# Kernel optimization log

Hardware: AMD Instinct MI355X
Metric: run time of the kernel (lower is better)

The kernel has to match this reference:

```python
import jax, jax.numpy as jnp
import numpy as np

N_NODES = 50000
N_EDGES = 800000
C_IN = 128
C_OUT = 64
C_HID = 2 * C_OUT  # 128


def setup_inputs() -> dict:
    key = jax.random.key(0)
    ks = jax.random.split(key, 8)
    x = jax.random.normal(ks[0], (N_NODES, C_IN), dtype=jnp.float32)
    edge_index = jax.random.randint(ks[1], (2, N_EDGES), 0, N_NODES, dtype=jnp.int64)
    s1 = 1.0 / np.sqrt(C_IN)
    s2 = 1.0 / np.sqrt(C_HID)
    s3 = 1.0 / np.sqrt(C_OUT)
    W1 = jax.random.uniform(ks[2], (C_IN, C_HID), jnp.float32, -s1, s1)
    b1 = jnp.zeros((C_HID,), jnp.float32)
    W2 = jax.random.uniform(ks[3], (C_HID, C_OUT), jnp.float32, -s2, s2)
    b2 = jnp.zeros((C_OUT,), jnp.float32)
    Wb = jax.random.uniform(ks[4], (1, C_OUT, C_OUT), jnp.float32, -s3, s3)
    bb = jax.random.uniform(ks[5], (1,), jnp.float32, -s3, s3)
    return {"x": x, "edge_index": edge_index, "W1": W1, "b1": b1,
            "W2": W2, "b2": b2, "Wb": Wb, "bb": bb}


def gcn_conv(x, W, b, src, dst, n_nodes):
    # PyG GCNConv: h = x @ W; add self-loops; symmetric normalization D^-1/2 (A+I) D^-1/2.
    h = x @ W  # [N, F]
    ones = jnp.ones((src.shape[0],), h.dtype)
    deg = jax.ops.segment_sum(ones, dst, num_segments=n_nodes) + 1.0  # +1 for self-loop
    dinv = jax.lax.rsqrt(deg)
    norm = dinv[src] * dinv[dst]  # [E]
    msgs = h[src] * norm[:, None]  # [E, F]
    agg = jax.ops.segment_sum(msgs, dst, num_segments=n_nodes)
    # self-loop contribution: norm_ii = 1/deg_i
    agg = agg + h * (1.0 / deg)[:, None]
    return agg + b


def reference(x, edge_index, W1, b1, W2, b2, Wb, bb):
    src = edge_index[0]
    dst = edge_index[1]
    n = x.shape[0]
    # encode
    h = jax.nn.relu(gcn_conv(x, W1, b1, src, dst, n))
    z = gcn_conv(h, W2, b2, src, dst, n)  # [N, C_OUT]
    # decode: bilinear on (z[src], z[dst]) -> sigmoid
    zs = z[src]  # [E, C_OUT]
    zd = z[dst]  # [E, C_OUT]
    logits = jnp.einsum('ec,ocd,ed->eo', zs, Wb, zd) + bb  # [E, 1]
    return jax.nn.sigmoid(logits)
```

## Files before the change

### kernel.cpp

```cpp
#include <hip/hip_runtime.h>
#include <hip/hip_bf16.h>


#define N_NODES 50000
#define BSH 7
#define BSZ 128
#define NBUCK ((N_NODES + BSZ - 1) / BSZ)
#define EPB 4096
#define CAP 3072

typedef unsigned int u32;
typedef unsigned short u16;

typedef __attribute__((ext_vector_type(8))) short bf16x8;
typedef __attribute__((ext_vector_type(4))) float f32x4;
union frag_u { bf16x8 f; u32 u[4]; uint4 v; };

__device__ __forceinline__ float bflo(u32 u) { return __uint_as_float(u << 16); }
__device__ __forceinline__ float bfhi(u32 u) { return __uint_as_float(u & 0xffff0000u); }
__device__ __forceinline__ u32 f2bf(float f) {
    u32 b = __float_as_uint(f);
    return (b + 0x7fffu + ((b >> 16) & 1u)) >> 16;
}
__device__ __forceinline__ u32 pack2(float a, float b) { return f2bf(a) | (f2bf(b) << 16); }

__global__ __launch_bounds__(256) void gemm1_scatter(
        const float* __restrict__ X, const float* __restrict__ W,
        u16* __restrict__ O, int n_rows, int gblk,
        const int* __restrict__ src, const int* __restrict__ dst,
        int* __restrict__ bcur, u32* __restrict__ pair, int E) {
    constexpr int K = 128, NOUT = 128;
    constexpr int KP = K + 8;
    constexpr int NT = NOUT / 16;
    constexpr int KS = K / 32;
    __shared__ __align__(16) char smem[NOUT * KP * 2 * sizeof(u16)];
    int t = threadIdx.x;

    if ((int)blockIdx.x < gblk) {
        u16* Wt_hi = (u16*)smem;
        u16* Wt_lo = Wt_hi + NOUT * KP;
        for (int i4 = t; i4 < K * NOUT / 4; i4 += 256) {
            int k = (i4 * 4) / NOUT;
            int n0 = (i4 * 4) % NOUT;
            float4 w4 = *(const float4*)&W[(size_t)k * NOUT + n0];
            float wv[4] = {w4.x, w4.y, w4.z, w4.w};
#pragma unroll
            for (int q = 0; q < 4; q++) {
                u32 hi = f2bf(wv[q]);
                u32 lo = f2bf(wv[q] - bflo(hi));
                Wt_hi[(n0 + q) * KP + k] = (u16)hi;
                Wt_lo[(n0 + q) * KP + k] = (u16)lo;
            }
        }
        __syncthreads();

        int wave = t >> 6;
        int lane = t & 63;
        int m16 = lane & 15;
        int quad = lane >> 4;
        int row0 = blockIdx.x * 128 + wave * 32;

        f32x4 acc[2][NT] = {};
        for (int ks = 0; ks < KS; ks++) {
            frag_u a_hi[2], a_lo[2];
#pragma unroll
            for (int mt = 0; mt < 2; mt++) {
                int row = row0 + mt * 16 + m16;
                row = row < n_rows ? row : n_rows - 1;
                const float* Xp = X + (size_t)row * K + ks * 32 + quad * 8;
                float4 x0 = *(const float4*)Xp;
                float4 x1 = *(const float4*)(Xp + 4);
                float xv[8] = {x0.x, x0.y, x0.z, x0.w, x1.x, x1.y, x1.z, x1.w};
#pragma unroll
                for (int p = 0; p < 4; p++) {
                    u32 h0 = f2bf(xv[2 * p]), h1 = f2bf(xv[2 * p + 1]);
                    a_hi[mt].u[p] = h0 | (h1 << 16);
                    a_lo[mt].u[p] = pack2(xv[2 * p] - bflo(h0), xv[2 * p + 1] - bflo(h1));
                }
            }
#pragma unroll
            for (int nt = 0; nt < NT; nt++) {
                int n = nt * 16 + m16;
                frag_u b_hi, b_lo;
                b_hi.v = *(const uint4*)&Wt_hi[n * KP + ks * 32 + quad * 8];
                b_lo.v = *(const uint4*)&Wt_lo[n * KP + ks * 32 + quad * 8];
#pragma unroll
                for (int mt = 0; mt < 2; mt++) {
                    acc[mt][nt] = __builtin_amdgcn_mfma_f32_16x16x32_bf16(a_hi[mt].f, b_hi.f, acc[mt][nt], 0, 0, 0);
                    acc[mt][nt] = __builtin_amdgcn_mfma_f32_16x16x32_bf16(a_hi[mt].f, b_lo.f, acc[mt][nt], 0, 0, 0);
                    acc[mt][nt] = __builtin_amdgcn_mfma_f32_16x16x32_bf16(a_lo[mt].f, b_hi.f, acc[mt][nt], 0, 0, 0);
                }
            }
        }
#pragma unroll
        for (int mt = 0; mt < 2; mt++)
#pragma unroll
            for (int nt = 0; nt < NT; nt++)
#pragma unroll
                for (int r = 0; r < 4; r++) {
                    int row = row0 + mt * 16 + quad * 4 + r;
                    if (row < n_rows)
                        O[(size_t)row * NOUT + nt * 16 + m16] = (u16)f2bf(acc[mt][nt][r]);
                }
    } else {
        int* hist = (int*)smem;
        for (int i = t; i < NBUCK; i += 256) hist[i] = 0;
        __syncthreads();
        int base = ((int)blockIdx.x - gblk) * EPB;
        int s_[16], d_[16];
#pragma unroll
        for (int it = 0; it < 16; it++) {
            int e = base + it * 256 + t;
            if (e < E) {
                s_[it] = src[e];
                d_[it] = dst[e];
                atomicAdd(&hist[d_[it] >> BSH], 1);
            } else {
                d_[it] = -1;
            }
        }
        __syncthreads();
        for (int b = t; b < NBUCK; b += 256) {
            int c = hist[b];
            hist[b] = c ? (b * CAP + atomicAdd(&bcur[b], c)) : 0;
        }
        __syncthreads();
#pragma unroll
        for (int it = 0; it < 16; it++) {
            if (d_[it] >= 0) {
                int b = d_[it] >> BSH;
                int off = atomicAdd(&hist[b], 1);
                pair[off] = (u32)s_[it] | ((u32)(d_[it] & (BSZ - 1)) << 16);
            }
        }
    }
}

__global__ __launch_bounds__(256) void bucket_sort(const u32* __restrict__ pair,
                                                   const int* __restrict__ bcur,
                                                   int* __restrict__ row_ptr,
                                                   int* __restrict__ col,
                                                   float* __restrict__ dinv,
                                                   float* __restrict__ inv, int n, int E) {
    __shared__ int ssum[256];
    __shared__ int cnt[BSZ];
    __shared__ int scn[BSZ];
    __shared__ int cur[BSZ];
    int t = threadIdx.x;
    int base = blockIdx.x << BSH;
    int nn = min(BSZ, n - base);
    int accp = 0;
    for (int i = t; i < (int)blockIdx.x; i += 256) accp += bcur[i];
    ssum[t] = accp;
    __syncthreads();
    for (int s = 128; s > 0; s >>= 1) {
        if (t < s) ssum[t] += ssum[t + s];
        __syncthreads();
    }
    int b0 = ssum[0];
    int cntE = bcur[blockIdx.x];
    int p0 = blockIdx.x * CAP;
    if (t < BSZ) cnt[t] = 0;
    __syncthreads();
    for (int j = t; j < cntE; j += 256)
        atomicAdd(&cnt[pair[p0 + j] >> 16], 1);
    __syncthreads();
    if (t < BSZ) scn[t] = cnt[t];
    __syncthreads();
    for (int off = 1; off < BSZ; off <<= 1) {
        int a = (t < BSZ && t >= off) ? scn[t - off] : 0;
        __syncthreads();
        if (t < BSZ) scn[t] += a;
        __syncthreads();
    }
    if (t < nn) {
        int excl = b0 + scn[t] - cnt[t];
        row_ptr[base + t] = excl;
        cur[t] = excl;
        float d = (float)cnt[t] + 1.0f;
        dinv[base + t] = rsqrtf(d);
        inv[base + t] = 1.0f / d;
    }
    if (t == 0 && blockIdx.x == NBUCK - 1) row_ptr[n] = E;
    __syncthreads();
    for (int j = t; j < cntE; j += 256) {
        u32 p = pair[p0 + j];
        int ln = (int)(p >> 16);
        int pos = atomicAdd(&cur[ln], 1);
        col[pos] = (int)(p & 0xffffu);
    }
}

template <int K, int NOUT>
__global__ __launch_bounds__(256) void gemm_mfma_bf(const u16* __restrict__ Xv,
                                                    const float* __restrict__ W,
                                                    u16* __restrict__ O, int n_rows) {
    constexpr int KP = K + 8;
    constexpr int NT = NOUT / 16;
    constexpr int KS = K / 32;
    __shared__ __align__(16) u16 Wt_hi[NOUT * KP];
    __shared__ __align__(16) u16 Wt_lo[NOUT * KP];
    int t = threadIdx.x;
    for (int i4 = t; i4 < K * NOUT / 4; i4 += 256) {
        int k = (i4 * 4) / NOUT;
        int n0 = (i4 * 4) % NOUT;
        float4 w4 = *(const float4*)&W[(size_t)k * NOUT + n0];
        float wv[4] = {w4.x, w4.y, w4.z, w4.w};
#pragma unroll
        for (int q = 0; q < 4; q++) {
            u32 hi = f2bf(wv[q]);
            u32 lo = f2bf(wv[q] - bflo(hi));
            Wt_hi[(n0 + q) * KP + k] = (u16)hi;
            Wt_lo[(n0 + q) * KP + k] = (u16)lo;
        }
    }
    __syncthreads();

    int wave = t >> 6;
    int lane = t & 63;
    int m16 = lane & 15;
    int quad = lane >> 4;
    int row0 = blockIdx.x * 128 + wave * 32;

    f32x4 acc[2][NT] = {};
    for (int ks = 0; ks < KS; ks++) {
        frag_u a_hi[2];
#pragma unroll
        for (int mt = 0; mt < 2; mt++) {
            int row = row0 + mt * 16 + m16;
            row = row < n_rows ? row : n_rows - 1;
            a_hi[mt].v = *(const uint4*)(Xv + (size_t)row * K + ks * 32 + quad * 8);
        }
#pragma unroll
        for (int nt = 0; nt < NT; nt++) {
            int n = nt * 16 + m16;
            frag_u b_hi, b_lo;
            b_hi.v = *(const uint4*)&Wt_hi[n * KP + ks * 32 + quad * 8];
            b_lo.v = *(const uint4*)&Wt_lo[n * KP + ks * 32 + quad * 8];
#pragma unroll
            for (int mt = 0; mt < 2; mt++) {
                acc[mt][nt] = __builtin_amdgcn_mfma_f32_16x16x32_bf16(a_hi[mt].f, b_hi.f, acc[mt][nt], 0, 0, 0);
                acc[mt][nt] = __builtin_amdgcn_mfma_f32_16x16x32_bf16(a_hi[mt].f, b_lo.f, acc[mt][nt], 0, 0, 0);
            }
        }
    }
#pragma unroll
    for (int mt = 0; mt < 2; mt++)
#pragma unroll
        for (int nt = 0; nt < NT; nt++)
#pragma unroll
            for (int r = 0; r < 4; r++) {
                int row = row0 + mt * 16 + quad * 4 + r;
                if (row < n_rows)
                    O[(size_t)row * NOUT + nt * 16 + m16] = (u16)f2bf(acc[mt][nt][r]);
            }
}

template <int C, bool RELU>
__global__ __launch_bounds__(256) void agg_pull(const u16* __restrict__ H,
                                                const int* __restrict__ row_ptr,
                                                const int* __restrict__ col,
                                                const float* __restrict__ dinv,
                                                const float* __restrict__ inv,
                                                const float* __restrict__ b,
                                                u16* __restrict__ O, int n) {
    constexpr int TPN = C / 8;
    const uint4* Hv = (const uint4*)H;
    int tid = blockIdx.x * 256 + threadIdx.x;
    int node = tid / TPN;
    if (node >= n) return;
    int part = tid % TPN;
    int c8 = part * 8;
    float dn = dinv[node];
    float iv = inv[node];
    float acc[8];
    {
        uint4 h = Hv[(size_t)node * TPN + part];
        acc[0] = bflo(h.x) * iv + b[c8 + 0];
        acc[1] = bfhi(h.x) * iv + b[c8 + 1];
        acc[2] = bflo(h.y) * iv + b[c8 + 2];
        acc[3] = bfhi(h.y) * iv + b[c8 + 3];
        acc[4] = bflo(h.z) * iv + b[c8 + 4];
        acc[5] = bfhi(h.z) * iv + b[c8 + 5];
        acc[6] = bflo(h.w) * iv + b[c8 + 6];
        acc[7] = bfhi(h.w) * iv + b[c8 + 7];
    }
    int j = row_ptr[node];
    int end = row_ptr[node + 1];
    for (; j + 3 < end; j += 4) {
        int s0 = col[j], s1 = col[j + 1], s2 = col[j + 2], s3 = col[j + 3];
        float n0 = dn * dinv[s0], n1 = dn * dinv[s1];
        float n2 = dn * dinv[s2], n3 = dn * dinv[s3];
        uint4 v0 = Hv[(size_t)s0 * TPN + part];
        uint4 v1 = Hv[(size_t)s1 * TPN + part];
        uint4 v2 = Hv[(size_t)s2 * TPN + part];
        uint4 v3 = Hv[(size_t)s3 * TPN + part];
        acc[0] += bflo(v0.x) * n0 + bflo(v1.x) * n1 + bflo(v2.x) * n2 + bflo(v3.x) * n3;
        acc[1] += bfhi(v0.x) * n0 + bfhi(v1.x) * n1 + bfhi(v2.x) * n2 + bfhi(v3.x) * n3;
        acc[2] += bflo(v0.y) * n0 + bflo(v1.y) * n1 + bflo(v2.y) * n2 + bflo(v3.y) * n3;
        acc[3] += bfhi(v0.y) * n0 + bfhi(v1.y) * n1 + bfhi(v2.y) * n2 + bfhi(v3.y) * n3;
        acc[4] += bflo(v0.z) * n0 + bflo(v1.z) * n1 + bflo(v2.z) * n2 + bflo(v3.z) * n3;
        acc[5] += bfhi(v0.z) * n0 + bfhi(v1.z) * n1 + bfhi(v2.z) * n2 + bfhi(v3.z) * n3;
        acc[6] += bflo(v0.w) * n0 + bflo(v1.w) * n1 + bflo(v2.w) * n2 + bflo(v3.w) * n3;
        acc[7] += bfhi(v0.w) * n0 + bfhi(v1.w) * n1 + bfhi(v2.w) * n2 + bfhi(v3.w) * n3;
    }
    for (; j < end; j++) {
        int s = col[j];
        float nm = dn * dinv[s];
        uint4 v = Hv[(size_t)s * TPN + part];
        acc[0] += bflo(v.x) * nm; acc[1] += bfhi(v.x) * nm;
        acc[2] += bflo(v.y) * nm; acc[3] += bfhi(v.y) * nm;
        acc[4] += bflo(v.z) * nm; acc[5] += bfhi(v.z) * nm;
        acc[6] += bflo(v.w) * nm; acc[7] += bfhi(v.w) * nm;
    }
    if (RELU) {
#pragma unroll
        for (int i = 0; i < 8; i++) acc[i] = fmaxf(acc[i], 0.f);
    }
    uint4 o;
    o.x = pack2(acc[0], acc[1]);
    o.y = pack2(acc[2], acc[3]);
    o.z = pack2(acc[4], acc[5]);
    o.w = pack2(acc[6], acc[7]);
    ((uint4*)O)[(size_t)node * TPN + part] = o;
}

__global__ __launch_bounds__(256) void decode_kernel(const u16* __restrict__ Y,
                                                     const u16* __restrict__ Z,
                                                     const int* __restrict__ src,
                                                     const int* __restrict__ dst,
                                                     const float* __restrict__ bb,
                                                     float* __restrict__ out, int E) {
    const uint4* Yv = (const uint4*)Y;
    const uint4* Zv = (const uint4*)Z;
    int tid = blockIdx.x * 256 + threadIdx.x;
    int e = tid / 8;
    int lane = tid % 8;
    if (e >= E) return;
    int s = src[e], d = dst[e];
    uint4 y = Yv[(size_t)s * 8 + lane];
    uint4 z = Zv[(size_t)d * 8 + lane];
    float p = bflo(y.x) * bflo(z.x) + bfhi(y.x) * bfhi(z.x)
            + bflo(y.y) * bflo(z.y) + bfhi(y.y) * bfhi(z.y)
            + bflo(y.z) * bflo(z.z) + bfhi(y.z) * bfhi(z.z)
            + bflo(y.w) * bflo(z.w) + bfhi(y.w) * bfhi(z.w);
    p += __shfl_down(p, 4, 8);
    p += __shfl_down(p, 2, 8);
    p += __shfl_down(p, 1, 8);
    if (lane == 0) out[e] = 1.0f / (1.0f + expf(-(p + bb[0])));
}

extern "C" void kernel_launch(void* const* d_in, const int* in_sizes, int n_in,
                              void* d_out, int out_size, void* d_ws, size_t ws_size,
                              hipStream_t stream) {
    const float* x  = (const float*)d_in[0];
    const int*   ei = (const int*)d_in[1];
    const float* W1 = (const float*)d_in[2];
    const float* b1 = (const float*)d_in[3];
    const float* W2 = (const float*)d_in[4];
    const float* b2 = (const float*)d_in[5];
    const float* Wb = (const float*)d_in[6];
    const float* bb = (const float*)d_in[7];
    float* out = (float*)d_out;

    const int N = N_NODES;
    const int E = in_sizes[1] / 2;
    const int* src = ei;
    const int* dst = ei + E;
    const int GBLK = (N + 127) / 128;
    const int SBLK = (E + EPB - 1) / EPB;

    char* w = (char*)d_ws;
    int*   bcur    = (int*)w;   w += (size_t)512 * 4;
    int*   row_ptr = (int*)w;   w += (size_t)(N + 1) * 4;
    int*   col     = (int*)w;   w += (size_t)E * 4;
    u32*   pair    = (u32*)w;   w += (size_t)NBUCK * CAP * 4;
    float* dinv    = (float*)w; w += (size_t)N * 4;
    float* inv     = (float*)w; w += (size_t)N * 4;
    w = (char*)(((size_t)w + 15) & ~(size_t)15);
    u16* bufA = (u16*)w;        w += (size_t)N * 128 * 2;
    u16* bufB = (u16*)w;        w += (size_t)N * 128 * 2;
    u16* bufC = (u16*)w;

    u16* H1 = bufA;
    u16* h1 = bufB;
    u16* H2 = bufA;
    u16* Z  = bufC;
    u16* Y  = bufA + (size_t)N * 64;

    hipMemsetAsync(bcur, 0, 512 * 4, stream);
    gemm1_scatter<<<GBLK + SBLK, 256, 0, stream>>>(x, W1, H1, N, GBLK,
                                                   src, dst, bcur, pair, E);
    bucket_sort<<<NBUCK, 256, 0, stream>>>(pair, bcur, row_ptr, col, dinv, inv, N, E);

    agg_pull<128, true><<<((size_t)N * 16 + 255) / 256, 256, 0, stream>>>(
        H1, row_ptr, col, dinv, inv, b1, h1, N);

    gemm_mfma_bf<128, 64><<<GBLK, 256, 0, stream>>>(h1, W2, H2, N);
    agg_pull<64, false><<<((size_t)N * 8 + 255) / 256, 256, 0, stream>>>(
        H2, row_ptr, col, dinv, inv, b2, Z, N);

    gemm_mfma_bf<64, 64><<<GBLK, 256, 0, stream>>>(Z, Wb, Y, N);
    decode_kernel<<<((size_t)E * 8 + 255) / 256, 256, 0, stream>>>(Y, Z, src, dst, bb, out, E);
}
```

Baseline: 238.9 us.

## Decode edges in dst-sorted CSR order to localize dst-side feature reads

The scatter now packs the original edge id into a 64-bit pair, and bucket_sort writes a per-CSR-slot eidx array holding that edge id and the local destination index. Decode walks edges bucket by bucket in CSR order. It computes Wb·z[dst] once per node (transposed-weight GEMM) and reads those dst rows from a small local window, then scatters each result back to its original edge position. The aim is better cache locality on the destination-side gather. In exchange, the pair buffer is twice as large, there is an extra eidx write and read per edge, and the output stores are scattered rather than coalesced.

```diff
diff --git a/kernel.cpp b/kernel.cpp
--- a/kernel.cpp
+++ b/kernel.cpp
@@ -8,9 +8,11 @@
 #define NBUCK ((N_NODES + BSZ - 1) / BSZ)
 #define EPB 4096
 #define CAP 3072
+#define DSPLIT 4
 
 typedef unsigned int u32;
 typedef unsigned short u16;
+typedef unsigned long long u64;
 
 typedef __attribute__((ext_vector_type(8))) short bf16x8;
 typedef __attribute__((ext_vector_type(4))) float f32x4;
@@ -28,7 +30,7 @@
         const float* __restrict__ X, const float* __restrict__ W,
         u16* __restrict__ O, int n_rows, int gblk,
         const int* __restrict__ src, const int* __restrict__ dst,
-        int* __restrict__ bcur, u32* __restrict__ pair, int E) {
+        int* __restrict__ bcur, u64* __restrict__ pair, int E) {
     constexpr int K = 128, NOUT = 128;
     constexpr int KP = K + 8;
     constexpr int NT = NOUT / 16;
@@ -130,16 +132,19 @@
             if (d_[it] >= 0) {
                 int b = d_[it] >> BSH;
                 int off = atomicAdd(&hist[b], 1);
-                pair[off] = (u32)s_[it] | ((u32)(d_[it] & (BSZ - 1)) << 16);
-            }
-        }
-    }
-}
-
-__global__ __launch_bounds__(256) void bucket_sort(const u32* __restrict__ pair,
+                int e = base + it * 256 + t;
+                pair[off] = (u64)((u32)s_[it] | ((u32)(d_[it] & (BSZ - 1)) << 16))
+                          | ((u64)(u32)e << 32);
+            }
+        }
+    }
+}
+
+__global__ __launch_bounds__(256) void bucket_sort(const u64* __restrict__ pair,
                                                    const int* __restrict__ bcur,
                                                    int* __restrict__ row_ptr,
                                                    int* __restrict__ col,
+                                                   u32* __restrict__ eidx,
                                                    float* __restrict__ dinv,
                                                    float* __restrict__ inv, int n, int E) {
     __shared__ int ssum[256];
@@ -163,7 +168,7 @@
     if (t < BSZ) cnt[t] = 0;
     __syncthreads();
     for (int j = t; j < cntE; j += 256)
-        atomicAdd(&cnt[pair[p0 + j] >> 16], 1);
+        atomicAdd(&cnt[(int)((pair[p0 + j] >> 16) & (BSZ - 1))], 1);
     __syncthreads();
     if (t < BSZ) scn[t] = cnt[t];
     __syncthreads();
@@ -184,14 +189,15 @@
     if (t == 0 && blockIdx.x == NBUCK - 1) row_ptr[n] = E;
     __syncthreads();
     for (int j = t; j < cntE; j += 256) {
-        u32 p = pair[p0 + j];
-        int ln = (int)(p >> 16);
+        u64 p = pair[p0 + j];
+        int ln = (int)((p >> 16) & (BSZ - 1));
         int pos = atomicAdd(&cur[ln], 1);
         col[pos] = (int)(p & 0xffffu);
-    }
-}
-
-template <int K, int NOUT>
+        eidx[pos] = (u32)(p >> 32) | ((u32)ln << 20);
+    }
+}
+
+template <int K, int NOUT, bool TRANSW>
 __global__ __launch_bounds__(256) void gemm_mfma_bf(const u16* __restrict__ Xv,
                                                     const float* __restrict__ W,
                                                     u16* __restrict__ O, int n_rows) {
@@ -202,16 +208,30 @@
     __shared__ __align__(16) u16 Wt_lo[NOUT * KP];
     int t = threadIdx.x;
     for (int i4 = t; i4 < K * NOUT / 4; i4 += 256) {
-        int k = (i4 * 4) / NOUT;
-        int n0 = (i4 * 4) % NOUT;
-        float4 w4 = *(const float4*)&W[(size_t)k * NOUT + n0];
-        float wv[4] = {w4.x, w4.y, w4.z, w4.w};
-#pragma unroll
-        for (int q = 0; q < 4; q++) {
-            u32 hi = f2bf(wv[q]);
-            u32 lo = f2bf(wv[q] - bflo(hi));
-            Wt_hi[(n0 + q) * KP + k] = (u16)hi;
-            Wt_lo[(n0 + q) * KP + k] = (u16)lo;
+        if constexpr (!TRANSW) {
+            int k = (i4 * 4) / NOUT;
+            int n0 = (i4 * 4) % NOUT;
+            float4 w4 = *(const float4*)&W[(size_t)k * NOUT + n0];
+            float wv[4] = {w4.x, w4.y, w4.z, w4.w};
+#pragma unroll
+            for (int q = 0; q < 4; q++) {
+                u32 hi = f2bf(wv[q]);
+                u32 lo = f2bf(wv[q] - bflo(hi));
+                Wt_hi[(n0 + q) * KP + k] = (u16)hi;
+                Wt_lo[(n0 + q) * KP + k] = (u16)lo;
+            }
+        } else {
+            int n = (i4 * 4) / K;
+            int k0 = (i4 * 4) % K;
+            float4 w4 = *(const float4*)&W[(size_t)n * K + k0];
+            float wv[4] = {w4.x, w4.y, w4.z, w4.w};
+#pragma unroll
+            for (int q = 0; q < 4; q++) {
+                u32 hi = f2bf(wv[q]);
+                u32 lo = f2bf(wv[q] - bflo(hi));
+                Wt_hi[n * KP + k0 + q] = (u16)hi;
+                Wt_lo[n * KP + k0 + q] = (u16)lo;
+            }
         }
     }
     __syncthreads();
@@ -325,29 +345,43 @@
     ((uint4*)O)[(size_t)node * TPN + part] = o;
 }
 
-__global__ __launch_bounds__(256) void decode_kernel(const u16* __restrict__ Y,
-                                                     const u16* __restrict__ Z,
-                                                     const int* __restrict__ src,
-                                                     const int* __restrict__ dst,
-                                                     const float* __restrict__ bb,
-                                                     float* __restrict__ out, int E) {
-    const uint4* Yv = (const uint4*)Y;
+__global__ __launch_bounds__(256) void decode_csr(const u16* __restrict__ Z,
+                                                  const u16* __restrict__ Q,
+                                                  const int* __restrict__ row_ptr,
+                                                  const int* __restrict__ col,
+                                                  const u32* __restrict__ eidx,
+                                                  const float* __restrict__ bb,
+                                                  float* __restrict__ out, int n) {
     const uint4* Zv = (const uint4*)Z;
-    int tid = blockIdx.x * 256 + threadIdx.x;
-    int e = tid / 8;
-    int lane = tid % 8;
-    if (e >= E) return;
-    int s = src[e], d = dst[e];
-    uint4 y = Yv[(size_t)s * 8 + lane];
-    uint4 z = Zv[(size_t)d * 8 + lane];
-    float p = bflo(y.x) * bflo(z.x) + bfhi(y.x) * bfhi(z.x)
-            + bflo(y.y) * bflo(z.y) + bfhi(y.y) * bfhi(z.y)
-            + bflo(y.z) * bflo(z.z) + bfhi(y.z) * bfhi(z.z)
-            + bflo(y.w) * bflo(z.w) + bfhi(y.w) * bfhi(z.w);
-    p += __shfl_down(p, 4, 8);
-    p += __shfl_down(p, 2, 8);
-    p += __shfl_down(p, 1, 8);
-    if (lane == 0) out[e] = 1.0f / (1.0f + expf(-(p + bb[0])));
+    const uint4* Qv = (const uint4*)Q;
+    int bucket = blockIdx.x / DSPLIT;
+    int part = blockIdx.x % DSPLIT;
+    int base = bucket << BSH;
+    int nn = min(BSZ, n - base);
+    int j0 = row_ptr[base];
+    int j1 = row_ptr[base + nn];
+    int cnt = j1 - j0;
+    int chunk = (cnt + DSPLIT - 1) / DSPLIT;
+    int s0 = j0 + part * chunk;
+    int s1 = min(s0 + chunk, j1);
+    float bbv = bb[0];
+    int lane = threadIdx.x & 7;
+    for (int j = s0 + ((int)threadIdx.x >> 3); j < s1; j += 32) {
+        int s = col[j];
+        u32 m = eidx[j];
+        int loc = (int)(m >> 20);
+        int eid = (int)(m & 0xfffffu);
+        uint4 z = Zv[(size_t)s * 8 + lane];
+        uint4 q = Qv[(size_t)(base + loc) * 8 + lane];
+        float p = bflo(z.x) * bflo(q.x) + bfhi(z.x) * bfhi(q.x)
+                + bflo(z.y) * bflo(q.y) + bfhi(z.y) * bfhi(q.y)
+                + bflo(z.z) * bflo(q.z) + bfhi(z.z) * bfhi(q.z)
+                + bflo(z.w) * bflo(q.w) + bfhi(z.w) * bfhi(q.w);
+        p += __shfl_down(p, 4, 8);
+        p += __shfl_down(p, 2, 8);
+        p += __shfl_down(p, 1, 8);
+        if (lane == 0) out[eid] = 1.0f / (1.0f + expf(-(p + bbv)));
+    }
 }
 
 extern "C" void kernel_launch(void* const* d_in, const int* in_sizes, int n_in,
@@ -374,7 +408,9 @@
     int*   bcur    = (int*)w;   w += (size_t)512 * 4;
     int*   row_ptr = (int*)w;   w += (size_t)(N + 1) * 4;
     int*   col     = (int*)w;   w += (size_t)E * 4;
-    u32*   pair    = (u32*)w;   w += (size_t)NBUCK * CAP * 4;
+    u32*   eidx    = (u32*)w;   w += (size_t)E * 4;
+    w = (char*)(((size_t)w + 15) & ~(size_t)15);
+    u64*   pair    = (u64*)w;   w += (size_t)NBUCK * CAP * 8;
     float* dinv    = (float*)w; w += (size_t)N * 4;
     float* inv     = (float*)w; w += (size_t)N * 4;
     w = (char*)(((size_t)w + 15) & ~(size_t)15);
@@ -386,20 +422,20 @@
     u16* h1 = bufB;
     u16* H2 = bufA;
     u16* Z  = bufC;
-    u16* Y  = bufA + (size_t)N * 64;
+    u16* Q  = bufA + (size_t)N * 64;
 
     hipMemsetAsync(bcur, 0, 512 * 4, stream);
     gemm1_scatter<<<GBLK + SBLK, 256, 0, stream>>>(x, W1, H1, N, GBLK,
                                                    src, dst, bcur, pair, E);
-    bucket_sort<<<NBUCK, 256, 0, stream>>>(pair, bcur, row_ptr, col, dinv, inv, N, E);
+    bucket_sort<<<NBUCK, 256, 0, stream>>>(pair, bcur, row_ptr, col, eidx, dinv, inv, N, E);
 
     agg_pull<128, true><<<((size_t)N * 16 + 255) / 256, 256, 0, stream>>>(
         H1, row_ptr, col, dinv, inv, b1, h1, N);
 
-    gemm_mfma_bf<128, 64><<<GBLK, 256, 0, stream>>>(h1, W2, H2, N);
+    gemm_mfma_bf<128, 64, false><<<GBLK, 256, 0, stream>>>(h1, W2, H2, N);
     agg_pull<64, false><<<((size_t)N * 8 + 255) / 256, 256, 0, stream>>>(
         H2, row_ptr, col, dinv, inv, b2, Z, N);
 
-    gemm_mfma_bf<64, 64><<<GBLK, 256, 0, stream>>>(Z, Wb, Y, N);
-    decode_kernel<<<((size_t)E * 8 + 255) / 256, 256, 0, stream>>>(Y, Z, src, dst, bb, out, E);
-}
+    gemm_mfma_bf<64, 64, true><<<GBLK, 256, 0, stream>>>(Z, Wb, Q, N);
+    decode_csr<<<NBUCK * DSPLIT, 256, 0, stream>>>(Z, Q, row_ptr, col, eidx, bb, out, N);
+}
```

Result: no change. 236.0 us (-1.2%).
